# Performance work log

Measured on AMD Instinct MI355X. Metric: run time of the kernel, lower is better.

Reference implementation:

```python
import jax, jax.numpy as jnp
import numpy as np

NEG = -1e9
BN_EPS = 1e-3  # keras BatchNormalization default epsilon
LRELU = 0.2    # GAT leaky-relu slope


def _gat(Xt, bias_mat, Wg, a1, a2, bg):
    """Dense multi-head GAT (Velickovic TF impl).
    Xt: [B,N,F], bias_mat: [B,N,N] additive mask (0 / -1e9).
    Wg: [H,F,D], a1/a2/bg: [H,D]. Returns [B,N,H*D]."""
    feats = jnp.einsum('bnf,hfd->bhnd', Xt, Wg)          # [B,H,N,D]
    f1 = jnp.einsum('bhnd,hd->bhn', feats, a1)
    f2 = jnp.einsum('bhnd,hd->bhn', feats, a2)
    logits = f1[:, :, :, None] + f2[:, :, None, :]        # [B,H,N,N]
    logits = jax.nn.leaky_relu(logits, LRELU) + bias_mat[:, None]
    coefs = jax.nn.softmax(logits, axis=-1)
    vals = jnp.einsum('bhnm,bhmd->bhnd', coefs, feats) + bg[None, :, None, :]
    vals = jax.nn.elu(vals)
    B, H, N, D = vals.shape
    return jnp.transpose(vals, (0, 2, 1, 3)).reshape(B, N, H * D)


def setup_inputs() -> dict:
    key = jax.random.key(0)
    ks = jax.random.split(key, 16)
    B, T, N, F = 4, 12, 2048, 64
    H, D = 4, 16           # attn_heads, hid_units
    C = H * D              # out_channels = 64

    X = jax.random.normal(ks[0], (B, T, N, F), dtype=jnp.float32)
    # random sparse adjacency (~avg degree 16) + self loops -> additive mask
    adj = jax.random.uniform(ks[1], (B, N, N)) < (16.0 / N)
    adj = adj | jnp.eye(N, dtype=bool)[None]
    bias_mat = jnp.where(adj, 0.0, NEG).astype(jnp.float32)

    he = lambda k, s: jax.random.normal(k, s, dtype=jnp.float32) * np.sqrt(2.0 / s[-2] if len(s) > 1 else 2.0 / s[-1])
    return {
        'X': X, 'bias_mat': bias_mat,
        'W_z': he(ks[2], (F, C)), 'Z_bias': he(ks[3], (1, C)),
        'W_h': he(ks[4], (F, C)), 'H_bias': he(ks[5], (1, C)),
        'Wg_z': he(ks[6], (H, F, D)), 'a1_z': he(ks[7], (H, D)),
        'a2_z': he(ks[8], (H, D)), 'bg_z': jnp.zeros((H, D), jnp.float32),
        'Wg_h': he(ks[9], (H, F, D)), 'a1_h': he(ks[10], (H, D)),
        'a2_h': he(ks[11], (H, D)), 'bg_h': jnp.zeros((H, D), jnp.float32),
        'bn_gamma': jnp.ones((C,), jnp.float32), 'bn_beta': jnp.zeros((C,), jnp.float32),
        'bn_mean': jnp.zeros((C,), jnp.float32), 'bn_var': jnp.ones((C,), jnp.float32),
    }


def reference(X, bias_mat, W_z, Z_bias, W_h, H_bias,
              Wg_z, a1_z, a2_z, bg_z, Wg_h, a1_h, a2_h, bg_h,
              bn_gamma, bn_beta, bn_mean, bn_var):
    B, T, N, F = X.shape
    C = W_z.shape[1]
    H0 = jnp.zeros((B, N, C), dtype=jnp.float32)

    def step(Hc, Xt):
        Z = _gat(Xt, bias_mat, Wg_z, a1_z, a2_z, bg_z) + Xt @ W_z + Z_bias + Hc
        Z = jax.nn.sigmoid(Z)
        Tt = _gat(Xt, bias_mat, Wg_h, a1_h, a2_h, bg_h) + Hc + Xt @ W_h + H_bias
        Tt = jnp.tanh(Tt)
        Hn = Z * Hc + (1.0 - Z) * Tt
        return Hn, None

    Xs = jnp.transpose(X, (1, 0, 2, 3))  # [T,B,N,F]
    Hf, _ = jax.lax.scan(step, H0, Xs)
    # last_layer=True path: BatchNorm (inference, moving stats) on final H
    out = (Hf - bn_mean) * jax.lax.rsqrt(bn_var + BN_EPS) * bn_gamma + bn_beta
    return out
```

## Files before the change

### kernel.cpp

```cpp
#include <hip/hip_runtime.h>
#include <cstdint>
#include <cstddef>

#define NB 4
#define NT 12
#define NN 2048
#define NF 64
#define NH 4
#define ND 16
#define NC 64
#define MAXD 64
#define NR (NB * NT * NN)

typedef _Float16 f16x8 __attribute__((ext_vector_type(8)));
typedef _Float16 f16x2 __attribute__((ext_vector_type(2)));
typedef float f32x4 __attribute__((ext_vector_type(4)));

#define LR(v) fmaxf((v), 0.2f * (v))
#define RCPF(x) __builtin_amdgcn_rcpf(x)

#define MACLO(acc, w, d)                                                      \
  asm("v_fma_mix_f32 %0, %1, %2, %0 op_sel:[0,0,0] op_sel_hi:[0,1,0]"         \
      : "+v"(acc) : "v"(w), "v"(d))
#define MACHI(acc, w, d)                                                      \
  asm("v_fma_mix_f32 %0, %1, %2, %0 op_sel:[0,1,0] op_sel_hi:[0,1,0]"         \
      : "+v"(acc) : "v"(w), "v"(d))

__global__ __launch_bounds__(256) void build_adj_k(const float* __restrict__ bias,
                                                   int* __restrict__ adj,
                                                   int* __restrict__ deg) {
  int gtid = blockIdx.x * 256 + threadIdx.x;
  int wid = gtid >> 6;
  int lane = threadIdx.x & 63;
  if (wid >= NB * NN) return;
  const float* row = bias + (size_t)wid * NN;
  int* arow = adj + (size_t)wid * MAXD;
  int count = 0;
  for (int c0 = 0; c0 < NN; c0 += 64) {
    float v = __builtin_nontemporal_load(row + c0 + lane);
    bool e = (v > -1e8f);
    unsigned long long m = __ballot(e);
    int pre = __popcll(m & ((1ull << lane) - 1ull));
    if (e) {
      int pos = count + pre;
      if (pos < MAXD) arow[pos] = c0 + lane;
    }
    count += __popcll(m);
  }
  if (lane == 0) deg[wid] = count < MAXD ? count : MAXD;
}

__global__ __launch_bounds__(256) void prep_w_k(
    const float* __restrict__ Wgz, const float* __restrict__ Wgh,
    const float* __restrict__ Wz,  const float* __restrict__ Wh,
    const float* __restrict__ a1z, const float* __restrict__ a2z,
    const float* __restrict__ a1h, const float* __restrict__ a2h,
    const float* __restrict__ Zb,  const float* __restrict__ Hb,
    _Float16* __restrict__ W16, float* __restrict__ biasC) {
  int idx = blockIdx.x * 256 + threadIdx.x;
  if (idx < 272 * 64) {
    int c = idx >> 6, k = idx & 63;
    float w;
    if (c < 64)       w = Wgz[((c >> 4) << 10) + (k << 4) + (c & 15)];
    else if (c < 128) { int q = c - 64; w = Wgh[((q >> 4) << 10) + (k << 4) + (q & 15)]; }
    else if (c < 192) w = Wz[(k << 6) + (c - 128)];
    else if (c < 256) w = Wh[(k << 6) + (c - 192)];
    else {
      int j = c - 256, h = j & 3;
      const float* Wg = (j & 4) ? Wgh : Wgz;
      const float* av = (j & 8) ? ((j & 4) ? a2h : a2z) : ((j & 4) ? a1h : a1z);
      float s = 0.f;
#pragma unroll
      for (int d = 0; d < 16; d++)
        s = fmaf(Wg[(h << 10) + (k << 4) + d], av[(h << 4) + d], s);
      w = s;
    }
    W16[idx] = (_Float16)w;
  }
  if (blockIdx.x == 0 && threadIdx.x < 128)
    biasC[threadIdx.x] =
        (threadIdx.x < 64) ? Zb[threadIdx.x] : Hb[threadIdx.x - 64];
}

__global__ __launch_bounds__(256) void mfma_gemm_k(
    const float* __restrict__ X, const _Float16* __restrict__ W16,
    const float* __restrict__ biasC,
    uint32_t* __restrict__ gbufF, uint32_t* __restrict__ gbufS,
    float* __restrict__ fbuf) {
  __shared__ uint32_t tr[4][16 * 68];
  const int tid = threadIdx.x;
  const int wv = tid >> 6, lane = tid & 63;
  const int m = lane & 15, quad = lane >> 4;
  const unsigned rw = blockIdx.x * 64 + wv * 16;
  uint32_t* tw = tr[wv];

  const float* xr = X + (size_t)(rw + m) * 64;
  float4 x0 = *(const float4*)(xr + quad * 8);
  float4 x1 = *(const float4*)(xr + quad * 8 + 4);
  float4 x2 = *(const float4*)(xr + 32 + quad * 8);
  float4 x3 = *(const float4*)(xr + 32 + quad * 8 + 4);
  f16x8 A0 = {(_Float16)x0.x, (_Float16)x0.y, (_Float16)x0.z, (_Float16)x0.w,
              (_Float16)x1.x, (_Float16)x1.y, (_Float16)x1.z, (_Float16)x1.w};
  f16x8 A1 = {(_Float16)x2.x, (_Float16)x2.y, (_Float16)x2.z, (_Float16)x2.w,
              (_Float16)x3.x, (_Float16)x3.y, (_Float16)x3.z, (_Float16)x3.w};

  float bzc[4], bhc[4];
#pragma unroll
  for (int j = 0; j < 4; j++) {
    bzc[j] = biasC[j * 16 + m];
    bhc[j] = biasC[64 + j * 16 + m];
  }
  const int rsub = lane >> 4, chk = lane & 15;

  f32x4 zacc[4], zs[4];
#pragma unroll
  for (int ct = 0; ct < 17; ct++) {
    const _Float16* wp = W16 + (ct * 16 + m) * 64;
    f16x8 B0 = *(const f16x8*)(wp + quad * 8);
    f16x8 B1 = *(const f16x8*)(wp + 32 + quad * 8);
    f32x4 acc = {0.f, 0.f, 0.f, 0.f};
    acc = __builtin_amdgcn_mfma_f32_16x16x32_f16(A0, B0, acc, 0, 0, 0);
    acc = __builtin_amdgcn_mfma_f32_16x16x32_f16(A1, B1, acc, 0, 0, 0);
    if (ct < 4) {
      zacc[ct] = acc;
    } else if (ct < 8) {
      const int j = ct - 4;
#pragma unroll
      for (int r = 0; r < 4; r++) {
        f16x2 pv = {(_Float16)zacc[j][r], (_Float16)acc[r]};
        tw[(quad * 4 + r) * 68 + j * 16 + m] = __builtin_bit_cast(uint32_t, pv);
      }
      if (ct == 7) {
#pragma unroll
        for (int i = 0; i < 4; i++) {
          int row = i * 4 + rsub;
          uint4 v = *(const uint4*)&tw[row * 68 + chk * 4];
          *(uint4*)&gbufF[(size_t)(rw + row) * 64 + chk * 4] = v;
        }
      }
    } else if (ct < 12) {
#pragma unroll
      for (int r = 0; r < 4; r++) zs[ct - 8][r] = acc[r] + bzc[ct - 8];
    } else if (ct < 16) {
      const int j = ct - 12;
#pragma unroll
      for (int r = 0; r < 4; r++) {
        f16x2 pv = {(_Float16)zs[j][r], (_Float16)(acc[r] + bhc[j])};
        tw[(quad * 4 + r) * 68 + j * 16 + m] = __builtin_bit_cast(uint32_t, pv);
      }
      if (ct == 15) {
#pragma unroll
        for (int i = 0; i < 4; i++) {
          int row = i * 4 + rsub;
          uint4 v = *(const uint4*)&tw[row * 68 + chk * 4];
          *(uint4*)&gbufS[(size_t)(rw + row) * 64 + chk * 4] = v;
        }
      }
    } else {
      const unsigned rb = rw + quad * 4;
#pragma unroll
      for (int r = 0; r < 4; r++) fbuf[(size_t)(rb + r) * 16 + m] = acc[r];
    }
  }
}

__global__ __launch_bounds__(256) void attn_k(
    const uint32_t* __restrict__ gbufF, const uint32_t* __restrict__ gbufS,
    const float* __restrict__ fbuf,
    const int* __restrict__ adj, const int* __restrict__ deg,
    const float* __restrict__ bgz, const float* __restrict__ bgh,
    uint32_t* __restrict__ abuf) {
  __shared__ int adjS[4][MAXD];
  __shared__ float wexp[4][8][68];
  const int tid = threadIdx.x;
  const int lane = tid & 63;
  const int ws = tid >> 6;
  const int node = blockIdx.x * 4 + ws;
  const int t = blockIdx.y;
  const int b = node >> 11;
  const int nl = node & (NN - 1);
  const int dg = deg[node];
  adjS[ws][lane] = (lane < dg) ? (adj[node * MAXD + lane] << 6) : 0;
  const int dgp = (dg + 3) & ~3;
  const int ch = lane, hh = lane >> 4;
  const int sr = lane & 7, ss = lane >> 3;

  const unsigned rb = (unsigned)(b * NT + t) * NN;
  const float* fb = fbuf + (size_t)rb * 16;
  const uint32_t* gF = gbufF + (size_t)rb * 64;
  const uint32_t spd = gbufS[((size_t)rb + nl) * 64 + ch];

  {
    const float4* p = (const float4*)(fb + nl * 16);
    float4 f1z = p[0], f1h = p[1];
    if (lane < dg) {
      const float4* q =
          (const float4*)((const char*)fb + (size_t)(unsigned)adjS[ws][lane]);
      float4 f2z = q[2], f2h = q[3];
      wexp[ws][0][lane] = __expf(LR(f1z.x + f2z.x));
      wexp[ws][1][lane] = __expf(LR(f1z.y + f2z.y));
      wexp[ws][2][lane] = __expf(LR(f1z.z + f2z.z));
      wexp[ws][3][lane] = __expf(LR(f1z.w + f2z.w));
      wexp[ws][4][lane] = __expf(LR(f1h.x + f2h.x));
      wexp[ws][5][lane] = __expf(LR(f1h.y + f2h.y));
      wexp[ws][6][lane] = __expf(LR(f1h.z + f2h.z));
      wexp[ws][7][lane] = __expf(LR(f1h.w + f2h.w));
    } else {
#pragma unroll
      for (int k = 0; k < 8; k++) wexp[ws][k][lane] = 0.f;
    }
  }

  float4 u0 = *(const float4*)&wexp[ws][sr][ss * 8];
  float4 u1 = *(const float4*)&wexp[ws][sr][ss * 8 + 4];
  float part = ((u0.x + u0.y) + (u0.z + u0.w)) +
               ((u1.x + u1.y) + (u1.z + u1.w));
  part += __shfl_xor(part, 8);
  part += __shfl_xor(part, 16);
  part += __shfl_xor(part, 32);
  const float rsz = RCPF(__shfl(part, hh));
  const float rsh = RCPF(__shfl(part, 4 + hh));

  float az = 0.f, ah = 0.f;
  const float* wz = wexp[ws][hh];
  const float* wh = wexp[ws][4 + hh];
  int mi = 0;
  for (; mi + 8 <= dgp; mi += 8) {
    int4 ma = *(const int4*)&adjS[ws][mi];
    int4 mb = *(const int4*)&adjS[ws][mi + 4];
    uint32_t d0 = gF[ma.x + ch];
    uint32_t d1 = gF[ma.y + ch];
    uint32_t d2 = gF[ma.z + ch];
    uint32_t d3 = gF[ma.w + ch];
    uint32_t d4 = gF[mb.x + ch];
    uint32_t d5 = gF[mb.y + ch];
    uint32_t d6 = gF[mb.z + ch];
    uint32_t d7 = gF[mb.w + ch];
    float4 wza = *(const float4*)&wz[mi];
    float4 wzb = *(const float4*)&wz[mi + 4];
    float4 wha = *(const float4*)&wh[mi];
    float4 whb = *(const float4*)&wh[mi + 4];
    MACLO(az, wza.x, d0); MACHI(ah, wha.x, d0);
    MACLO(az, wza.y, d1); MACHI(ah, wha.y, d1);
    MACLO(az, wza.z, d2); MACHI(ah, wha.z, d2);
    MACLO(az, wza.w, d3); MACHI(ah, wha.w, d3);
    MACLO(az, wzb.x, d4); MACHI(ah, whb.x, d4);
    MACLO(az, wzb.y, d5); MACHI(ah, whb.y, d5);
    MACLO(az, wzb.z, d6); MACHI(ah, whb.z, d6);
    MACLO(az, wzb.w, d7); MACHI(ah, whb.w, d7);
  }
  if (mi < dgp) {
    int4 ma = *(const int4*)&adjS[ws][mi];
    uint32_t d0 = gF[ma.x + ch];
    uint32_t d1 = gF[ma.y + ch];
    uint32_t d2 = gF[ma.z + ch];
    uint32_t d3 = gF[ma.w + ch];
    float4 wza = *(const float4*)&wz[mi];
    float4 wha = *(const float4*)&wh[mi];
    MACLO(az, wza.x, d0); MACHI(ah, wha.x, d0);
    MACLO(az, wza.y, d1); MACHI(ah, wha.y, d1);
    MACLO(az, wza.z, d2); MACHI(ah, wha.z, d2);
    MACLO(az, wza.w, d3); MACHI(ah, wha.w, d3);
  }
  az *= rsz;
  ah *= rsh;

  f16x2 sp = __builtin_bit_cast(f16x2, spd);
  float vz = az + bgz[ch]; vz = vz > 0.f ? vz : __expf(vz) - 1.f;
  float vh = ah + bgh[ch]; vh = vh > 0.f ? vh : __expf(vh) - 1.f;
  f16x2 pre = {(_Float16)(vz + (float)sp.x), (_Float16)(vh + (float)sp.y)};
  abuf[(size_t)(rb + nl) * 64 + ch] = __builtin_bit_cast(uint32_t, pre);
}

__global__ __launch_bounds__(256) void gru_k(
    const uint32_t* __restrict__ abuf,
    const float* __restrict__ gam, const float* __restrict__ bet,
    const float* __restrict__ mu, const float* __restrict__ var,
    float* __restrict__ out) {
  const int gtid = blockIdx.x * 256 + threadIdx.x;
  const int node = gtid >> 6, ch = gtid & 63;
  const int b = node >> 11, nl = node & (NN - 1);
  float hc = 0.f;
#pragma unroll
  for (int t = 0; t < NT; t++) {
    f16x2 pre = __builtin_bit_cast(
        f16x2, abuf[(size_t)((b * NT + t) * NN + nl) * 64 + ch]);
    float zg = RCPF(1.f + __expf(-((float)pre.x + hc)));
    float ta = (float)pre.y + hc;
    float tg = 1.f - 2.f * RCPF(__expf(2.f * ta) + 1.f);
    hc = zg * hc + (1.f - zg) * tg;
  }
  out[gtid] = (hc - mu[ch]) * rsqrtf(var[ch] + 1e-3f) * gam[ch] + bet[ch];
}

extern "C" void kernel_launch(void* const* d_in, const int* in_sizes, int n_in,
                              void* d_out, int out_size, void* d_ws, size_t ws_size,
                              hipStream_t stream) {
  (void)in_sizes; (void)n_in; (void)out_size; (void)ws_size;
  const float* X   = (const float*)d_in[0];
  const float* bm  = (const float*)d_in[1];
  const float* Wz  = (const float*)d_in[2];
  const float* Zb  = (const float*)d_in[3];
  const float* Wh  = (const float*)d_in[4];
  const float* Hb  = (const float*)d_in[5];
  const float* Wgz = (const float*)d_in[6];
  const float* a1z = (const float*)d_in[7];
  const float* a2z = (const float*)d_in[8];
  const float* bgz = (const float*)d_in[9];
  const float* Wgh = (const float*)d_in[10];
  const float* a1h = (const float*)d_in[11];
  const float* a2h = (const float*)d_in[12];
  const float* bgh = (const float*)d_in[13];
  const float* gam = (const float*)d_in[14];
  const float* bet = (const float*)d_in[15];
  const float* mu  = (const float*)d_in[16];
  const float* var = (const float*)d_in[17];
  float* out = (float*)d_out;

  char* p = (char*)d_ws;
  uint32_t* gbufF = (uint32_t*)p; p += (size_t)NR * 64 * sizeof(uint32_t);
  uint32_t* gbufS = (uint32_t*)p; p += (size_t)NR * 64 * sizeof(uint32_t);
  float*    fbuf  = (float*)p;    p += (size_t)NR * 16 * sizeof(float);
  uint32_t* abuf  = (uint32_t*)p; p += (size_t)NR * 64 * sizeof(uint32_t);
  int*      adj   = (int*)p;      p += (size_t)NB * NN * MAXD * sizeof(int);
  int*      deg   = (int*)p;      p += (size_t)NB * NN * sizeof(int);
  _Float16* W16   = (_Float16*)p; p += 272 * 64 * sizeof(_Float16);
  float*    biasC = (float*)p;    p += 128 * sizeof(float);

  prep_w_k<<<dim3(68), dim3(256), 0, stream>>>(
      Wgz, Wgh, Wz, Wh, a1z, a2z, a1h, a2h, Zb, Hb, W16, biasC);
  build_adj_k<<<dim3(NB * NN / 4), dim3(256), 0, stream>>>(bm, adj, deg);
  mfma_gemm_k<<<dim3(NR / 64), dim3(256), 0, stream>>>(
      X, W16, biasC, gbufF, gbufS, fbuf);
  attn_k<<<dim3(NB * NN / 4, NT), dim3(256), 0, stream>>>(
      gbufF, gbufS, fbuf, adj, deg, bgz, bgh, abuf);
  gru_k<<<dim3(NB * NN * 64 / 256), dim3(256), 0, stream>>>(
      abuf, gam, bet, mu, var, out);
}
```

Before: 240.8 us.

## Merge weight prep into adjacency kernel, interleave attention blocks by batch, use byte offsets

Folds the weight-packing kernel into the adjacency-building launch as extra blocks, which removes one kernel launch. The attention kernel now remaps block indices so that neighbouring blocks work on different batches, spreading gather traffic across the batch slices. Adjacency indices are stored pre-scaled to byte offsets, so the gather address becomes a plain byte add instead of an index shift. The block remap changes which blocks share the L2 cache, and that could hurt locality as easily as help it.

Result: faster. 233.8 us (-2.9%).

```diff
diff --git a/kernel.cpp b/kernel.cpp
--- a/kernel.cpp
+++ b/kernel.cpp
@@ -26,13 +26,43 @@
   asm("v_fma_mix_f32 %0, %1, %2, %0 op_sel:[0,1,0] op_sel_hi:[0,1,0]"         \
       : "+v"(acc) : "v"(w), "v"(d))
 
-__global__ __launch_bounds__(256) void build_adj_k(const float* __restrict__ bias,
-                                                   int* __restrict__ adj,
-                                                   int* __restrict__ deg) {
+__global__ __launch_bounds__(256) void build_adj_k(
+    const float* __restrict__ bias, int* __restrict__ adj, int* __restrict__ deg,
+    const float* __restrict__ Wgz, const float* __restrict__ Wgh,
+    const float* __restrict__ Wz,  const float* __restrict__ Wh,
+    const float* __restrict__ a1z, const float* __restrict__ a2z,
+    const float* __restrict__ a1h, const float* __restrict__ a2h,
+    const float* __restrict__ Zb,  const float* __restrict__ Hb,
+    _Float16* __restrict__ W16, float* __restrict__ biasC) {
+  if (blockIdx.x >= NB * NN / 4) {
+    int idx = (blockIdx.x - NB * NN / 4) * 256 + threadIdx.x;
+    if (idx < 272 * 64) {
+      int c = idx >> 6, k = idx & 63;
+      float w;
+      if (c < 64)       w = Wgz[((c >> 4) << 10) + (k << 4) + (c & 15)];
+      else if (c < 128) { int q = c - 64; w = Wgh[((q >> 4) << 10) + (k << 4) + (q & 15)]; }
+      else if (c < 192) w = Wz[(k << 6) + (c - 128)];
+      else if (c < 256) w = Wh[(k << 6) + (c - 192)];
+      else {
+        int j = c - 256, h = j & 3;
+        const float* Wg = (j & 4) ? Wgh : Wgz;
+        const float* av = (j & 8) ? ((j & 4) ? a2h : a2z) : ((j & 4) ? a1h : a1z);
+        float s = 0.f;
+#pragma unroll
+        for (int d = 0; d < 16; d++)
+          s = fmaf(Wg[(h << 10) + (k << 4) + d], av[(h << 4) + d], s);
+        w = s;
+      }
+      W16[idx] = (_Float16)w;
+    }
+    if (blockIdx.x == NB * NN / 4 && threadIdx.x < 128)
+      biasC[threadIdx.x] =
+          (threadIdx.x < 64) ? Zb[threadIdx.x] : Hb[threadIdx.x - 64];
+    return;
+  }
   int gtid = blockIdx.x * 256 + threadIdx.x;
   int wid = gtid >> 6;
   int lane = threadIdx.x & 63;
-  if (wid >= NB * NN) return;
   const float* row = bias + (size_t)wid * NN;
   int* arow = adj + (size_t)wid * MAXD;
   int count = 0;
@@ -50,38 +80,6 @@
   if (lane == 0) deg[wid] = count < MAXD ? count : MAXD;
 }
 
-__global__ __launch_bounds__(256) void prep_w_k(
-    const float* __restrict__ Wgz, const float* __restrict__ Wgh,
-    const float* __restrict__ Wz,  const float* __restrict__ Wh,
-    const float* __restrict__ a1z, const float* __restrict__ a2z,
-    const float* __restrict__ a1h, const float* __restrict__ a2h,
-    const float* __restrict__ Zb,  const float* __restrict__ Hb,
-    _Float16* __restrict__ W16, float* __restrict__ biasC) {
-  int idx = blockIdx.x * 256 + threadIdx.x;
-  if (idx < 272 * 64) {
-    int c = idx >> 6, k = idx & 63;
-    float w;
-    if (c < 64)       w = Wgz[((c >> 4) << 10) + (k << 4) + (c & 15)];
-    else if (c < 128) { int q = c - 64; w = Wgh[((q >> 4) << 10) + (k << 4) + (q & 15)]; }
-    else if (c < 192) w = Wz[(k << 6) + (c - 128)];
-    else if (c < 256) w = Wh[(k << 6) + (c - 192)];
-    else {
-      int j = c - 256, h = j & 3;
-      const float* Wg = (j & 4) ? Wgh : Wgz;
-      const float* av = (j & 8) ? ((j & 4) ? a2h : a2z) : ((j & 4) ? a1h : a1z);
-      float s = 0.f;
-#pragma unroll
-      for (int d = 0; d < 16; d++)
-        s = fmaf(Wg[(h << 10) + (k << 4) + d], av[(h << 4) + d], s);
-      w = s;
-    }
-    W16[idx] = (_Float16)w;
-  }
-  if (blockIdx.x == 0 && threadIdx.x < 128)
-    biasC[threadIdx.x] =
-        (threadIdx.x < 64) ? Zb[threadIdx.x] : Hb[threadIdx.x - 64];
-}
-
 __global__ __launch_bounds__(256) void mfma_gemm_k(
     const float* __restrict__ X, const _Float16* __restrict__ W16,
     const float* __restrict__ biasC,
@@ -175,27 +173,31 @@
   const int tid = threadIdx.x;
   const int lane = tid & 63;
   const int ws = tid >> 6;
-  const int node = blockIdx.x * 4 + ws;
+  const int bid = blockIdx.x;
+  const int g = bid & 7;
+  const int b = g >> 1;
+  const int grp = (bid >> 3) * 2 + (g & 1);
+  const int nl = grp * 4 + ws;
+  const int node = b * NN + nl;
   const int t = blockIdx.y;
-  const int b = node >> 11;
-  const int nl = node & (NN - 1);
   const int dg = deg[node];
-  adjS[ws][lane] = (lane < dg) ? (adj[node * MAXD + lane] << 6) : 0;
+  adjS[ws][lane] = (lane < dg) ? (adj[node * MAXD + lane] << 8) : 0;
   const int dgp = (dg + 3) & ~3;
   const int ch = lane, hh = lane >> 4;
+  const uint32_t ch4 = (uint32_t)ch << 2;
   const int sr = lane & 7, ss = lane >> 3;
 
   const unsigned rb = (unsigned)(b * NT + t) * NN;
   const float* fb = fbuf + (size_t)rb * 16;
-  const uint32_t* gF = gbufF + (size_t)rb * 64;
+  const char* gFc = (const char*)(gbufF + (size_t)rb * 64);
   const uint32_t spd = gbufS[((size_t)rb + nl) * 64 + ch];
 
   {
     const float4* p = (const float4*)(fb + nl * 16);
     float4 f1z = p[0], f1h = p[1];
     if (lane < dg) {
-      const float4* q =
-          (const float4*)((const char*)fb + (size_t)(unsigned)adjS[ws][lane]);
+      const float4* q = (const float4*)((const char*)fb +
+                                        ((unsigned)adjS[ws][lane] >> 2));
       float4 f2z = q[2], f2h = q[3];
       wexp[ws][0][lane] = __expf(LR(f1z.x + f2z.x));
       wexp[ws][1][lane] = __expf(LR(f1z.y + f2z.y));
@@ -228,14 +230,14 @@
   for (; mi + 8 <= dgp; mi += 8) {
     int4 ma = *(const int4*)&adjS[ws][mi];
     int4 mb = *(const int4*)&adjS[ws][mi + 4];
-    uint32_t d0 = gF[ma.x + ch];
-    uint32_t d1 = gF[ma.y + ch];
-    uint32_t d2 = gF[ma.z + ch];
-    uint32_t d3 = gF[ma.w + ch];
-    uint32_t d4 = gF[mb.x + ch];
-    uint32_t d5 = gF[mb.y + ch];
-    uint32_t d6 = gF[mb.z + ch];
-    uint32_t d7 = gF[mb.w + ch];
+    uint32_t d0 = *(const uint32_t*)(gFc + ((uint32_t)ma.x + ch4));
+    uint32_t d1 = *(const uint32_t*)(gFc + ((uint32_t)ma.y + ch4));
+    uint32_t d2 = *(const uint32_t*)(gFc + ((uint32_t)ma.z + ch4));
+    uint32_t d3 = *(const uint32_t*)(gFc + ((uint32_t)ma.w + ch4));
+    uint32_t d4 = *(const uint32_t*)(gFc + ((uint32_t)mb.x + ch4));
+    uint32_t d5 = *(const uint32_t*)(gFc + ((uint32_t)mb.y + ch4));
+    uint32_t d6 = *(const uint32_t*)(gFc + ((uint32_t)mb.z + ch4));
+    uint32_t d7 = *(const uint32_t*)(gFc + ((uint32_t)mb.w + ch4));
     float4 wza = *(const float4*)&wz[mi];
     float4 wzb = *(const float4*)&wz[mi + 4];
     float4 wha = *(const float4*)&wh[mi];
@@ -251,10 +253,10 @@
   }
   if (mi < dgp) {
     int4 ma = *(const int4*)&adjS[ws][mi];
-    uint32_t d0 = gF[ma.x + ch];
-    uint32_t d1 = gF[ma.y + ch];
-    uint32_t d2 = gF[ma.z + ch];
-    uint32_t d3 = gF[ma.w + ch];
+    uint32_t d0 = *(const uint32_t*)(gFc + ((uint32_t)ma.x + ch4));
+    uint32_t d1 = *(const uint32_t*)(gFc + ((uint32_t)ma.y + ch4));
+    uint32_t d2 = *(const uint32_t*)(gFc + ((uint32_t)ma.z + ch4));
+    uint32_t d3 = *(const uint32_t*)(gFc + ((uint32_t)ma.w + ch4));
     float4 wza = *(const float4*)&wz[mi];
     float4 wha = *(const float4*)&wh[mi];
     MACLO(az, wza.x, d0); MACHI(ah, wha.x, d0);
@@ -327,9 +329,8 @@
   _Float16* W16   = (_Float16*)p; p += 272 * 64 * sizeof(_Float16);
   float*    biasC = (float*)p;    p += 128 * sizeof(float);
 
-  prep_w_k<<<dim3(68), dim3(256), 0, stream>>>(
-      Wgz, Wgh, Wz, Wh, a1z, a2z, a1h, a2h, Zb, Hb, W16, biasC);
-  build_adj_k<<<dim3(NB * NN / 4), dim3(256), 0, stream>>>(bm, adj, deg);
+  build_adj_k<<<dim3(NB * NN / 4 + 68), dim3(256), 0, stream>>>(
+      bm, adj, deg, Wgz, Wgh, Wz, Wh, a1z, a2z, a1h, a2h, Zb, Hb, W16, biasC);
   mfma_gemm_k<<<dim3(NR / 64), dim3(256), 0, stream>>>(
       X, W16, biasC, gbufF, gbufS, fbuf);
   attn_k<<<dim3(NB * NN / 4, NT), dim3(256), 0, stream>>>(
```
